# Optimization experiments

Hardware: AMD Instinct MI355X
Metric: run time of the kernel (lower is better)

The kernel has to match this reference:

```python
import jax, jax.numpy as jnp
import numpy as np


def setup_inputs() -> dict:
    key = jax.random.key(0)
    k1, k2, k3 = jax.random.split(key, 3)
    B, t_dim, h_dim = 32, 256, 512
    h, w, M = 64, 64, 128
    H = jax.random.normal(k1, (B, h_dim, h, w), dtype=jnp.float32)
    W = jax.random.normal(k2, (B, t_dim, M), dtype=jnp.float32)
    # 1x1 conv weight [h_dim, t_dim, 1, 1] collapses to a [h_dim, t_dim] matmul
    head_w = jax.random.normal(k3, (h_dim, t_dim), dtype=jnp.float32) * (t_dim ** -0.5)
    return {"H": H, "W": W, "head_w": head_w}


def reference(H, W, head_w):
    S = H.shape                                   # [B, h_dim, h, w]
    Hf = H.reshape(S[0], S[1], -1)                # [B, h_dim, N]
    Wp = jnp.einsum('ht,btm->bhm', head_w, W)     # 1x1 conv proj: [B, h_dim, M]
    scores = jnp.einsum('bhn,bhm->bnm', Hf, Wp)   # [B, N, M]
    A = jax.nn.softmax(scores, axis=2)            # softmax over words M
    C = jnp.einsum('bnm,bhm->bnh', A, Wp)         # [B, N, h_dim]
    C = jnp.transpose(C, (0, 2, 1))               # [B, h_dim, N]
    return C.reshape(S)
```

## Files before the change

### kernel.cpp

```cpp
#include <hip/hip_runtime.h>

#define BB 32
#define TD 256
#define HD 512
#define MM 128
#define NN 4096

typedef __attribute__((ext_vector_type(8))) short short8;
typedef __attribute__((ext_vector_type(4))) float floatx4;

__device__ inline unsigned int bf16_rne(float f) {
    unsigned int u = __float_as_uint(f);
    return (u + 0x7fffu + ((u >> 16) & 1u)) >> 16;
}
__device__ inline float quad16_max(float v) {
    v = fmaxf(v, __shfl_xor(v, 1));
    v = fmaxf(v, __shfl_xor(v, 2));
    v = fmaxf(v, __shfl_xor(v, 4));
    v = fmaxf(v, __shfl_xor(v, 8));
    return v;
}
__device__ inline float quad16_sum(float v) {
    v += __shfl_xor(v, 1);
    v += __shfl_xor(v, 2);
    v += __shfl_xor(v, 4);
    v += __shfl_xor(v, 8);
    return v;
}

__global__ __launch_bounds__(256, 2) void wp_kernel(
    const float* __restrict__ Wmat,
    const float* __restrict__ head_w,
    unsigned short* __restrict__ Wpt_hi,
    unsigned short* __restrict__ Wpt_lo,
    unsigned short* __restrict__ Wp_b)
{
    const int tid = threadIdx.x;
    const int tx = tid & 31;
    const int ty = tid >> 5;
    const int b  = blockIdx.y;
    const int h0 = blockIdx.x * 64;

    __shared__ float s_hw[64][64];
    __shared__ float s_w[64][128];

    float acc[8][4];
#pragma unroll
    for (int r = 0; r < 8; ++r)
#pragma unroll
        for (int c = 0; c < 4; ++c) acc[r][c] = 0.f;

    for (int t0 = 0; t0 < TD; t0 += 64) {
#pragma unroll
        for (int k = 0; k < 4; ++k) {
            int i = (tid >> 4) + 16 * k;
            int j = (tid & 15) * 4;
            *(float4*)&s_hw[i][j] = *(const float4*)&head_w[(h0 + i) * TD + t0 + j];
        }
#pragma unroll
        for (int k = 0; k < 8; ++k) {
            int i = (tid >> 5) + 8 * k;
            *(float4*)&s_w[i][(tid & 31) * 4] =
                *(const float4*)&Wmat[((b * TD) + t0 + i) * MM + (tid & 31) * 4];
        }
        __syncthreads();
#pragma unroll 4
        for (int tt = 0; tt < 64; ++tt) {
            float b4[4];
            *(float4*)b4 = *(const float4*)&s_w[tt][tx * 4];
#pragma unroll
            for (int r = 0; r < 8; ++r) {
                float a = s_hw[ty * 8 + r][tt];
#pragma unroll
                for (int c = 0; c < 4; ++c) acc[r][c] += a * b4[c];
            }
        }
        __syncthreads();
    }

#pragma unroll
    for (int r = 0; r < 8; ++r) {
        unsigned int p0 = bf16_rne(acc[r][0]) | (bf16_rne(acc[r][1]) << 16);
        unsigned int p1 = bf16_rne(acc[r][2]) | (bf16_rne(acc[r][3]) << 16);
        uint2 v; v.x = p0; v.y = p1;
        *(uint2*)&Wp_b[((size_t)(b * HD) + h0 + ty * 8 + r) * MM + tx * 4] = v;
    }
#pragma unroll
    for (int c = 0; c < 4; ++c) {
        unsigned int hw4[4], lw4[4];
#pragma unroll
        for (int rp = 0; rp < 4; ++rp) {
            float x0 = acc[2 * rp][c], x1 = acc[2 * rp + 1][c];
            unsigned int u0 = __float_as_uint(x0), u1 = __float_as_uint(x1);
            float l0 = x0 - __uint_as_float(u0 & 0xffff0000u);
            float l1 = x1 - __uint_as_float(u1 & 0xffff0000u);
            hw4[rp] = (u0 >> 16) | (u1 & 0xffff0000u);
            lw4[rp] = bf16_rne(l0) | (bf16_rne(l1) << 16);
        }
        size_t base = ((size_t)(b * MM) + tx * 4 + c) * HD + h0 + ty * 8;
        *(uint4*)&Wpt_hi[base] = make_uint4(hw4[0], hw4[1], hw4[2], hw4[3]);
        *(uint4*)&Wpt_lo[base] = make_uint4(lw4[0], lw4[1], lw4[2], lw4[3]);
    }
}

__global__ __launch_bounds__(256, 2) void fused_kernel(
    const float* __restrict__ H,
    const unsigned short* __restrict__ Wpt_hi,
    const unsigned short* __restrict__ Wpt_lo,
    const unsigned short* __restrict__ Wp_b,
    float* __restrict__ out)
{
    __shared__ __align__(16) unsigned char smem[65536];
    const int tid = threadIdx.x;
    const int w   = tid >> 6;
    const int L   = tid & 63;
    const int q   = L >> 4;
    const int l15 = L & 15;
    const int b   = blockIdx.y;
    const int n0  = blockIdx.x * 128;

    unsigned char* Ah = smem;
    unsigned char* Al = smem + 16384;
    unsigned char* Bh = smem + 32768;
    unsigned char* Bl = smem + 49152;

    const int nh = (w & 1) * 64;
    const int mh = (w >> 1) * 64;

    const float* Hb = H + ((size_t)b * HD) * NN + n0;
    const unsigned short* WptH = Wpt_hi + (size_t)b * MM * HD;
    const unsigned short* WptL = Wpt_lo + (size_t)b * MM * HD;

    floatx4 acc[4][4];
#pragma unroll
    for (int nt = 0; nt < 4; ++nt)
#pragma unroll
        for (int mt = 0; mt < 4; ++mt) acc[nt][mt] = (floatx4){0.f, 0.f, 0.f, 0.f};

    const int sa_n = (w & 1) * 64 + (tid & 63);
    const int sa_h = (w >> 1) * 32;

    for (int hc = 0; hc < 8; ++hc) {
        const int h0 = hc * 64;
#pragma unroll
        for (int ii = 0; ii < 4; ++ii) {
            const int hh = sa_h + ii * 8;
            const float* src = Hb + (size_t)(h0 + hh) * NN + sa_n;
            unsigned int hp[4], lp[4];
#pragma unroll
            for (int jp = 0; jp < 4; ++jp) {
                float x0 = src[(size_t)(2 * jp) * NN];
                float x1 = src[(size_t)(2 * jp + 1) * NN];
                unsigned int u0 = __float_as_uint(x0), u1 = __float_as_uint(x1);
                float l0 = x0 - __uint_as_float(u0 & 0xffff0000u);
                float l1 = x1 - __uint_as_float(u1 & 0xffff0000u);
                hp[jp] = (u0 >> 16) | (u1 & 0xffff0000u);
                lp[jp] = bf16_rne(l0) | (bf16_rne(l1) << 16);
            }
            const int off = sa_n * 128 + (((hh >> 3) ^ (sa_n & 7)) * 16);
            *(uint4*)(Ah + off) = make_uint4(hp[0], hp[1], hp[2], hp[3]);
            *(uint4*)(Al + off) = make_uint4(lp[0], lp[1], lp[2], lp[3]);
        }
#pragma unroll
        for (int k = 0; k < 4; ++k) {
            int flat = tid + 256 * k;
            int m = flat >> 3, u = flat & 7;
            size_t g = (size_t)m * HD + h0 + u * 8;
            uint4 vh = *(const uint4*)&WptH[g];
            uint4 vl = *(const uint4*)&WptL[g];
            int off = m * 128 + ((u ^ (m & 7)) * 16);
            *(uint4*)(Bh + off) = vh;
            *(uint4*)(Bl + off) = vl;
        }
        __syncthreads();
#pragma unroll
        for (int ks = 0; ks < 2; ++ks) {
            short8 ahf[4], alf[4], bhf[4], blf[4];
#pragma unroll
            for (int nt = 0; nt < 4; ++nt) {
                int n = nh + nt * 16 + l15;
                int off = n * 128 + (((q + 4 * ks) ^ (n & 7)) * 16);
                ahf[nt] = *(short8*)(Ah + off);
                alf[nt] = *(short8*)(Al + off);
            }
#pragma unroll
            for (int mt = 0; mt < 4; ++mt) {
                int m = mh + mt * 16 + l15;
                int off = m * 128 + (((q + 4 * ks) ^ (m & 7)) * 16);
                bhf[mt] = *(short8*)(Bh + off);
                blf[mt] = *(short8*)(Bl + off);
            }
#pragma unroll
            for (int nt = 0; nt < 4; ++nt)
#pragma unroll
                for (int mt = 0; mt < 4; ++mt) {
                    acc[nt][mt] = __builtin_amdgcn_mfma_f32_16x16x32_bf16(ahf[nt], bhf[mt], acc[nt][mt], 0, 0, 0);
                    acc[nt][mt] = __builtin_amdgcn_mfma_f32_16x16x32_bf16(alf[nt], bhf[mt], acc[nt][mt], 0, 0, 0);
                    acc[nt][mt] = __builtin_amdgcn_mfma_f32_16x16x32_bf16(ahf[nt], blf[mt], acc[nt][mt], 0, 0, 0);
                }
        }
        __syncthreads();
    }

    float* redmax = (float*)(smem + 49152);
    float* redsum = (float*)(smem + 49152 + 1024);
    const int mhalf = w >> 1;

    float rmax[4][4];
#pragma unroll
    for (int nt = 0; nt < 4; ++nt)
#pragma unroll
        for (int r = 0; r < 4; ++r) {
            float v = fmaxf(fmaxf(acc[nt][0][r], acc[nt][1][r]),
                            fmaxf(acc[nt][2][r], acc[nt][3][r]));
            rmax[nt][r] = quad16_max(v);
        }
    if (l15 == 0) {
#pragma unroll
        for (int nt = 0; nt < 4; ++nt)
#pragma unroll
            for (int r = 0; r < 4; ++r)
                redmax[mhalf * 128 + nh + nt * 16 + q * 4 + r] = rmax[nt][r];
    }
    __syncthreads();
    float gmax[4][4], rsum[4][4];
#pragma unroll
    for (int nt = 0; nt < 4; ++nt)
#pragma unroll
        for (int r = 0; r < 4; ++r) {
            gmax[nt][r] = fmaxf(rmax[nt][r],
                                redmax[(1 - mhalf) * 128 + nh + nt * 16 + q * 4 + r]);
            float s = 0.f;
#pragma unroll
            for (int mt = 0; mt < 4; ++mt) {
                float e = __expf(acc[nt][mt][r] - gmax[nt][r]);
                acc[nt][mt][r] = e;
                s += e;
            }
            rsum[nt][r] = quad16_sum(s);
        }
    if (l15 == 0) {
#pragma unroll
        for (int nt = 0; nt < 4; ++nt)
#pragma unroll
            for (int r = 0; r < 4; ++r)
                redsum[mhalf * 128 + nh + nt * 16 + q * 4 + r] = rsum[nt][r];
    }
    __syncthreads();

    unsigned char* As = smem;
#pragma unroll
    for (int nt = 0; nt < 4; ++nt)
#pragma unroll
        for (int r = 0; r < 4; ++r) {
            int n = nh + nt * 16 + q * 4 + r;
            float inv = 1.f / (rsum[nt][r] + redsum[(1 - mhalf) * 128 + n]);
#pragma unroll
            for (int mt = 0; mt < 4; ++mt) {
                int m = mh + mt * 16 + l15;
                unsigned short v = (unsigned short)bf16_rne(acc[nt][mt][r] * inv);
                *(unsigned short*)(As + n * 256 + (((m >> 3) ^ (n & 15)) * 16) + (m & 7) * 2) = v;
            }
        }
    __syncthreads();

    const int hq = (w >> 1) * 32;
    unsigned char* Wpb = smem + 32768;
    const unsigned short* WpB = Wp_b + (size_t)b * HD * MM;
    float* outb = out + ((size_t)b * HD) * NN + n0;

    short8 af[4][4];
#pragma unroll
    for (int nt = 0; nt < 4; ++nt)
#pragma unroll
        for (int ks = 0; ks < 4; ++ks) {
            int n = nh + nt * 16 + l15;
            af[nt][ks] = *(short8*)(As + n * 256 + (((q + 4 * ks) ^ (n & 15)) * 16));
        }

    for (int hc = 0; hc < 8; ++hc) {
#pragma unroll
        for (int k = 0; k < 4; ++k) {
            int flat = tid + 256 * k;
            int hrow = flat >> 4, u = flat & 15;
            uint4 v = *(const uint4*)&WpB[(size_t)(hc * 64 + hrow) * MM + u * 8];
            *(uint4*)(Wpb + hrow * 256 + ((u ^ (hrow & 15)) * 16)) = v;
        }
        __syncthreads();

        floatx4 accB[4][2];
#pragma unroll
        for (int nt = 0; nt < 4; ++nt)
#pragma unroll
            for (int ht = 0; ht < 2; ++ht) accB[nt][ht] = (floatx4){0.f, 0.f, 0.f, 0.f};

#pragma unroll
        for (int ks = 0; ks < 4; ++ks) {
            short8 bf[2];
#pragma unroll
            for (int ht = 0; ht < 2; ++ht) {
                int hl = hq + ht * 16 + l15;
                bf[ht] = *(short8*)(Wpb + hl * 256 + (((q + 4 * ks) ^ (hl & 15)) * 16));
            }
#pragma unroll
            for (int nt = 0; nt < 4; ++nt)
#pragma unroll
                for (int ht = 0; ht < 2; ++ht)
                    accB[nt][ht] = __builtin_amdgcn_mfma_f32_16x16x32_bf16(af[nt][ks], bf[ht], accB[nt][ht], 0, 0, 0);
        }
#pragma unroll
        for (int nt = 0; nt < 4; ++nt)
#pragma unroll
            for (int ht = 0; ht < 2; ++ht) {
                int hglob = hc * 64 + hq + ht * 16 + l15;
                int nrow = nh + nt * 16 + q * 4;
                *(floatx4*)(outb + (size_t)hglob * NN + nrow) = accB[nt][ht];
            }
        __syncthreads();
    }
}

extern "C" void kernel_launch(void* const* d_in, const int* in_sizes, int n_in,
                              void* d_out, int out_size, void* d_ws, size_t ws_size,
                              hipStream_t stream)
{
    (void)in_sizes; (void)n_in; (void)out_size; (void)ws_size;
    const float* H      = (const float*)d_in[0];
    const float* Wmat   = (const float*)d_in[1];
    const float* head_w = (const float*)d_in[2];
    float* out = (float*)d_out;

    unsigned short* Wpt_hi = (unsigned short*)d_ws;
    unsigned short* Wpt_lo = Wpt_hi + (size_t)BB * MM * HD;
    unsigned short* Wp_b   = Wpt_lo + (size_t)BB * MM * HD;

    wp_kernel<<<dim3(HD / 64, BB), 256, 0, stream>>>(Wmat, head_w, Wpt_hi, Wpt_lo, Wp_b);
    fused_kernel<<<dim3(NN / 128, BB), 256, 0, stream>>>(H, Wpt_hi, Wpt_lo, Wp_b, out);
}
```

Baseline: 486.2 us.

## Double-buffer both GEMM phases with async global-to-LDS loads and register prefetch

Restructures the fused kernel's score GEMM into 16 half-depth chunks with ping-pong LDS buffers. Wp tiles are loaded directly into LDS via global_load_lds, and the next chunk's H values are prefetched into registers while the current chunk's MFMAs run. The output GEMM also double-buffers Wp_b tiles with async LDS loads and counted vmcnt waits, which removes one barrier per iteration, and setprio is raised around the MFMA block. This hides global load latency behind compute, at the cost of more registers (16 prefetched floats) and more fragile hand-written wait counts.

```diff
diff --git a/kernel.cpp b/kernel.cpp
--- a/kernel.cpp
+++ b/kernel.cpp
@@ -26,6 +26,13 @@
     v += __shfl_xor(v, 4);
     v += __shfl_xor(v, 8);
     return v;
+}
+
+__device__ __forceinline__ void gload16(const void* gptr, void* ldsptr) {
+    __builtin_amdgcn_global_load_lds(
+        (const __attribute__((address_space(1))) void*)gptr,
+        (__attribute__((address_space(3))) void*)ldsptr,
+        16, 0, 0);
 }
 
 __global__ __launch_bounds__(256, 2) void wp_kernel(
@@ -119,11 +126,6 @@
     const int b   = blockIdx.y;
     const int n0  = blockIdx.x * 128;
 
-    unsigned char* Ah = smem;
-    unsigned char* Al = smem + 16384;
-    unsigned char* Bh = smem + 32768;
-    unsigned char* Bl = smem + 49152;
-
     const int nh = (w & 1) * 64;
     const int mh = (w >> 1) * 64;
 
@@ -137,73 +139,105 @@
 #pragma unroll
         for (int mt = 0; mt < 4; ++mt) acc[nt][mt] = (floatx4){0.f, 0.f, 0.f, 0.f};
 
-    const int sa_n = (w & 1) * 64 + (tid & 63);
-    const int sa_h = (w >> 1) * 32;
-
-    for (int hc = 0; hc < 8; ++hc) {
-        const int h0 = hc * 64;
-#pragma unroll
-        for (int ii = 0; ii < 4; ++ii) {
-            const int hh = sa_h + ii * 8;
-            const float* src = Hb + (size_t)(h0 + hh) * NN + sa_n;
+    const int sa_n = (w & 1) * 64 + L;
+    const int sa_h = (w >> 1) * 16;
+    const int u0   = (w >> 1) * 2;
+
+    int aw_off[2];
+#pragma unroll
+    for (int ii = 0; ii < 2; ++ii)
+        aw_off[ii] = sa_n * 64 + (((u0 + ii) ^ (sa_n & 3)) * 16);
+
+    int bg_off[2];
+#pragma unroll
+    for (int k = 0; k < 2; ++k) {
+        int flat = tid + 256 * k;
+        int m = flat >> 2, uu = flat & 3;
+        bg_off[k] = m * HD + ((uu ^ (m & 3)) * 8);
+    }
+    const int wave_lds = (tid & 192) * 16;
+
+    float xa[16];
+    const float* srcA = Hb + (size_t)sa_h * NN + sa_n;
+
+#pragma unroll
+    for (int k = 0; k < 2; ++k) {
+        gload16(WptH + bg_off[k], smem + 32768 + wave_lds + 256 * 16 * k);
+        gload16(WptL + bg_off[k], smem + 49152 + wave_lds + 256 * 16 * k);
+    }
+#pragma unroll
+    for (int t = 0; t < 16; ++t) xa[t] = srcA[(size_t)t * NN];
+
+#pragma unroll 1
+    for (int c = 0; c < 16; ++c) {
+        const int p = c & 1;
+        unsigned char* AhP = smem + p * 8192;
+        unsigned char* AlP = smem + 16384 + p * 8192;
+
+#pragma unroll
+        for (int ii = 0; ii < 2; ++ii) {
             unsigned int hp[4], lp[4];
 #pragma unroll
             for (int jp = 0; jp < 4; ++jp) {
-                float x0 = src[(size_t)(2 * jp) * NN];
-                float x1 = src[(size_t)(2 * jp + 1) * NN];
-                unsigned int u0 = __float_as_uint(x0), u1 = __float_as_uint(x1);
-                float l0 = x0 - __uint_as_float(u0 & 0xffff0000u);
-                float l1 = x1 - __uint_as_float(u1 & 0xffff0000u);
-                hp[jp] = (u0 >> 16) | (u1 & 0xffff0000u);
+                float x0 = xa[ii * 8 + 2 * jp], x1 = xa[ii * 8 + 2 * jp + 1];
+                unsigned int v0 = __float_as_uint(x0), v1 = __float_as_uint(x1);
+                float l0 = x0 - __uint_as_float(v0 & 0xffff0000u);
+                float l1 = x1 - __uint_as_float(v1 & 0xffff0000u);
+                hp[jp] = (v0 >> 16) | (v1 & 0xffff0000u);
                 lp[jp] = bf16_rne(l0) | (bf16_rne(l1) << 16);
             }
-            const int off = sa_n * 128 + (((hh >> 3) ^ (sa_n & 7)) * 16);
-            *(uint4*)(Ah + off) = make_uint4(hp[0], hp[1], hp[2], hp[3]);
-            *(uint4*)(Al + off) = make_uint4(lp[0], lp[1], lp[2], lp[3]);
-        }
-#pragma unroll
-        for (int k = 0; k < 4; ++k) {
-            int flat = tid + 256 * k;
-            int m = flat >> 3, u = flat & 7;
-            size_t g = (size_t)m * HD + h0 + u * 8;
-            uint4 vh = *(const uint4*)&WptH[g];
-            uint4 vl = *(const uint4*)&WptL[g];
-            int off = m * 128 + ((u ^ (m & 7)) * 16);
-            *(uint4*)(Bh + off) = vh;
-            *(uint4*)(Bl + off) = vl;
-        }
-        __syncthreads();
-#pragma unroll
-        for (int ks = 0; ks < 2; ++ks) {
-            short8 ahf[4], alf[4], bhf[4], blf[4];
-#pragma unroll
-            for (int nt = 0; nt < 4; ++nt) {
-                int n = nh + nt * 16 + l15;
-                int off = n * 128 + (((q + 4 * ks) ^ (n & 7)) * 16);
-                ahf[nt] = *(short8*)(Ah + off);
-                alf[nt] = *(short8*)(Al + off);
-            }
+            *(uint4*)(AhP + aw_off[ii]) = make_uint4(hp[0], hp[1], hp[2], hp[3]);
+            *(uint4*)(AlP + aw_off[ii]) = make_uint4(lp[0], lp[1], lp[2], lp[3]);
+        }
+        asm volatile("s_waitcnt vmcnt(0) lgkmcnt(0)" ::: "memory");
+        __builtin_amdgcn_s_barrier();
+        __builtin_amdgcn_sched_barrier(0);
+
+        if (c + 1 < 16) {
+            const int h0n = 32 * (c + 1);
+            unsigned char* BhN = smem + 32768 + (p ^ 1) * 8192;
+            unsigned char* BlN = smem + 49152 + (p ^ 1) * 8192;
+#pragma unroll
+            for (int k = 0; k < 2; ++k) {
+                gload16(WptH + h0n + bg_off[k], BhN + wave_lds + 256 * 16 * k);
+                gload16(WptL + h0n + bg_off[k], BlN + wave_lds + 256 * 16 * k);
+            }
+            srcA += (size_t)32 * NN;
+#pragma unroll
+            for (int t = 0; t < 16; ++t) xa[t] = srcA[(size_t)t * NN];
+        }
+
+        const unsigned char* BhP = smem + 32768 + p * 8192;
+        const unsigned char* BlP = smem + 49152 + p * 8192;
+        short8 ahf[4], alf[4], bhf[4], blf[4];
+#pragma unroll
+        for (int nt = 0; nt < 4; ++nt) {
+            int n = nh + nt * 16 + l15;
+            int off = n * 64 + ((q ^ (n & 3)) * 16);
+            ahf[nt] = *(const short8*)(AhP + off);
+            alf[nt] = *(const short8*)(AlP + off);
+        }
+#pragma unroll
+        for (int mt = 0; mt < 4; ++mt) {
+            int m = mh + mt * 16 + l15;
+            int off = m * 64 + ((q ^ (m & 3)) * 16);
+            bhf[mt] = *(const short8*)(BhP + off);
+            blf[mt] = *(const short8*)(BlP + off);
+        }
+        __builtin_amdgcn_s_setprio(1);
+#pragma unroll
+        for (int nt = 0; nt < 4; ++nt)
 #pragma unroll
             for (int mt = 0; mt < 4; ++mt) {
-                int m = mh + mt * 16 + l15;
-                int off = m * 128 + (((q + 4 * ks) ^ (m & 7)) * 16);
-                bhf[mt] = *(short8*)(Bh + off);
-                blf[mt] = *(short8*)(Bl + off);
-            }
-#pragma unroll
-            for (int nt = 0; nt < 4; ++nt)
-#pragma unroll
-                for (int mt = 0; mt < 4; ++mt) {
-                    acc[nt][mt] = __builtin_amdgcn_mfma_f32_16x16x32_bf16(ahf[nt], bhf[mt], acc[nt][mt], 0, 0, 0);
-                    acc[nt][mt] = __builtin_amdgcn_mfma_f32_16x16x32_bf16(alf[nt], bhf[mt], acc[nt][mt], 0, 0, 0);
-                    acc[nt][mt] = __builtin_amdgcn_mfma_f32_16x16x32_bf16(ahf[nt], blf[mt], acc[nt][mt], 0, 0, 0);
-                }
-        }
-        __syncthreads();
-    }
-
-    float* redmax = (float*)(smem + 49152);
-    float* redsum = (float*)(smem + 49152 + 1024);
+                acc[nt][mt] = __builtin_amdgcn_mfma_f32_16x16x32_bf16(ahf[nt], bhf[mt], acc[nt][mt], 0, 0, 0);
+                acc[nt][mt] = __builtin_amdgcn_mfma_f32_16x16x32_bf16(alf[nt], bhf[mt], acc[nt][mt], 0, 0, 0);
+                acc[nt][mt] = __builtin_amdgcn_mfma_f32_16x16x32_bf16(ahf[nt], blf[mt], acc[nt][mt], 0, 0, 0);
+            }
+        __builtin_amdgcn_s_setprio(0);
+    }
+
+    float* redmax = (float*)(smem + 32768);
+    float* redsum = (float*)(smem + 32768 + 1024);
     const int mhalf = w >> 1;
 
     float rmax[4][4];
@@ -265,9 +299,19 @@
     __syncthreads();
 
     const int hq = (w >> 1) * 32;
-    unsigned char* Wpb = smem + 32768;
     const unsigned short* WpB = Wp_b + (size_t)b * HD * MM;
     float* outb = out + ((size_t)b * HD) * NN + n0;
+
+    int wg_off[4];
+#pragma unroll
+    for (int k = 0; k < 4; ++k) {
+        int flat = tid + 256 * k;
+        int hrow = flat >> 4, uu = flat & 15;
+        wg_off[k] = hrow * MM + ((uu ^ (hrow & 15)) * 8);
+    }
+#pragma unroll
+    for (int k = 0; k < 4; ++k)
+        gload16(WpB + wg_off[k], smem + 32768 + wave_lds + 256 * 16 * k);
 
     short8 af[4][4];
 #pragma unroll
@@ -278,16 +322,23 @@
             af[nt][ks] = *(short8*)(As + n * 256 + (((q + 4 * ks) ^ (n & 15)) * 16));
         }
 
+#pragma unroll 1
     for (int hc = 0; hc < 8; ++hc) {
-#pragma unroll
-        for (int k = 0; k < 4; ++k) {
-            int flat = tid + 256 * k;
-            int hrow = flat >> 4, u = flat & 15;
-            uint4 v = *(const uint4*)&WpB[(size_t)(hc * 64 + hrow) * MM + u * 8];
-            *(uint4*)(Wpb + hrow * 256 + ((u ^ (hrow & 15)) * 16)) = v;
-        }
-        __syncthreads();
-
+        const int p = hc & 1;
+        if (hc == 0) { asm volatile("s_waitcnt vmcnt(0)" ::: "memory"); }
+        else         { asm volatile("s_waitcnt vmcnt(8)" ::: "memory"); }
+        __builtin_amdgcn_sched_barrier(0);
+        __builtin_amdgcn_s_barrier();
+        __builtin_amdgcn_sched_barrier(0);
+        if (hc + 1 < 8) {
+            const unsigned short* Wsrc = WpB + (size_t)(hc + 1) * 64 * MM;
+            unsigned char* WbN = smem + 32768 + (p ^ 1) * 16384;
+#pragma unroll
+            for (int k = 0; k < 4; ++k)
+                gload16(Wsrc + wg_off[k], WbN + wave_lds + 256 * 16 * k);
+        }
+
+        const unsigned char* WbP = smem + 32768 + p * 16384;
         floatx4 accB[4][2];
 #pragma unroll
         for (int nt = 0; nt < 4; ++nt)
@@ -300,7 +351,7 @@
 #pragma unroll
             for (int ht = 0; ht < 2; ++ht) {
                 int hl = hq + ht * 16 + l15;
-                bf[ht] = *(short8*)(Wpb + hl * 256 + (((q + 4 * ks) ^ (hl & 15)) * 16));
+                bf[ht] = *(const short8*)(WbP + hl * 256 + (((q + 4 * ks) ^ (hl & 15)) * 16));
             }
 #pragma unroll
             for (int nt = 0; nt < 4; ++nt)
@@ -316,7 +367,6 @@
                 int nrow = nh + nt * 16 + q * 4;
                 *(floatx4*)(outb + (size_t)hglob * NN + nrow) = accB[nt][ht];
             }
-        __syncthreads();
     }
 }
 
```

Measured after the change: 489.6 us. About the same (+0.7%).
